# Performance work log

Measured on AMD Instinct MI355X. Metric: run time of the kernel, lower is better.

Reference implementation:

```python
import jax, jax.numpy as jnp
import numpy as np

WIN = 7
NP_ = WIN * WIN
COV_NORM = NP_ / (NP_ - 1)

def _box(x, w):
    # valid 7x7 box filter, NCHW, single channel
    return jax.lax.conv_general_dilated(
        x, w, window_strides=(1, 1), padding='VALID',
        dimension_numbers=('NCHW', 'OIHW', 'NCHW'))

def setup_inputs() -> dict:
    key = jax.random.key(0)
    k1, k2, k3, k4 = jax.random.split(key, 4)
    N, H, W = 64, 384, 384
    X = jax.random.uniform(k1, (N, 1, H, W), dtype=jnp.float32)
    Y = jax.random.uniform(k2, (N, 1, H, W), dtype=jnp.float32)
    norm = jax.random.uniform(k3, (N,), dtype=jnp.float32)
    mx = jax.random.uniform(k4, (N,), dtype=jnp.float32) + 0.5
    w = jnp.ones((1, 1, WIN, WIN), dtype=jnp.float32) / NP_
    return {"X": X, "Y": Y, "norm": norm, "max": mx, "w": w}

def reference(X, Y, norm, max, w):
    q = 100000.0
    X = X * q
    Y = Y * q
    mx = max * q
    data_range = mx[:, None, None, None]
    C1 = (0.01 * data_range) ** 2
    C2 = (0.03 * data_range) ** 2
    ux = _box(X, w)
    uy = _box(Y, w)
    uxx = _box(X * X, w)
    uyy = _box(Y * Y, w)
    uxy = _box(X * Y, w)
    vx = COV_NORM * (uxx - ux * ux)
    vy = COV_NORM * (uyy - uy * uy)
    vxy = COV_NORM * (uxy - ux * uy)
    A1 = 2 * ux * uy + C1
    A2 = 2 * vxy + C2
    B1 = ux ** 2 + uy ** 2 + C1
    B2 = vx + vy + C2
    S = (A1 * A2) / (B1 * B2)
    return -jnp.mean(S)
```

## Files before the change

### kernel.cpp

```cpp
#include <hip/hip_runtime.h>


constexpr int IND   = 384;
constexpr int OUTD  = 378;
constexpr int RB    = 14;
constexpr int BANDS = OUTD / RB;
constexpr int CPL   = 6;

using f32x2 = __attribute__((ext_vector_type(2))) float;

#define FMA2(a, b, c) __builtin_elementwise_fma((a), (b), (c))

__global__ __launch_bounds__(64, 2)
void ssim_band(const float* __restrict__ X, const float* __restrict__ Y,
               const float* __restrict__ MX, float* __restrict__ blocksum)
{
    const int band = blockIdx.x;
    const int n    = blockIdx.y;
    const int lane = threadIdx.x;
    const int c0   = lane * CPL;
    const int r0   = band * RB;

    const float* __restrict__ Xp = X + (size_t)n * (IND * IND) + c0;
    const float* __restrict__ Yp = Y + (size_t)n * (IND * IND) + c0;

    f32x2 hx[7][3], hy[7][3];
    f32x2 sx[3]  = {}, sy[3]  = {};
    f32x2 sxx[3] = {}, syy[3] = {}, sxy[3] = {};

#define LOADROW(DX, DY, R) {                                                  \
    const float* _px = Xp + (size_t)(R) * IND;                                \
    const float* _py = Yp + (size_t)(R) * IND;                                \
    DX[0] = *(const f32x2*)_px;                                               \
    DX[1] = *(const f32x2*)(_px + 2);                                         \
    DX[2] = *(const f32x2*)(_px + 4);                                         \
    DY[0] = *(const f32x2*)_py;                                               \
    DY[1] = *(const f32x2*)(_py + 2);                                         \
    DY[2] = *(const f32x2*)(_py + 4); }

#pragma unroll
    for (int k = 0; k < 7; ++k) LOADROW(hx[k], hy[k], r0 + k)

    f32x2 pax[3], pay[3], pbx[3], pby[3];
    LOADROW(pax, pay, r0 + 7)
    LOADROW(pbx, pby, r0 + 8)

#pragma unroll
    for (int k = 0; k < 7; ++k)
#pragma unroll
        for (int g = 0; g < 3; ++g) {
            f32x2 x = hx[k][g], y = hy[k][g];
            sx[g] += x;  sy[g] += y;
            sxx[g] = FMA2(x, x, sxx[g]);
            syy[g] = FMA2(y, y, syy[g]);
            sxy[g] = FMA2(x, y, sxy[g]);
        }

    const float m   = MX[n];
    const float c1s = (0.01f * m) * (0.01f * m);
    const float c2s = (0.03f * m) * (0.03f * m);
    const float k1  = 2401.0f * c1s;
    const float k2  = 2401.0f * c2s;
    const f32x2 K1  = {k1, k1};
    const f32x2 K2  = {k2, k2};
    const f32x2 CN  = {49.0f / 48.0f, 49.0f / 48.0f};
    const f32x2 CN2 = {2.0f * 49.0f / 48.0f, 2.0f * 49.0f / 48.0f};
    const f32x2 TWO = {2.0f, 2.0f};
    const f32x2 F49 = {49.0f, 49.0f};

#define EL(S, c) (((c) & 1) ? S[(c) >> 1].y : S[(c) >> 1].x)

#define HSUM(S, O) {                                                          \
    float _n0 = __shfl_down(EL(S,0), 1), _n1 = __shfl_down(EL(S,1), 1);       \
    float _n2 = __shfl_down(EL(S,2), 1), _n3 = __shfl_down(EL(S,3), 1);       \
    float _n4 = __shfl_down(EL(S,4), 1), _n5 = __shfl_down(EL(S,5), 1);       \
    float _t  = ((EL(S,0)+EL(S,1)) + (EL(S,2)+EL(S,3))) + (EL(S,4)+EL(S,5));  \
    O[0] = _t   + _n0;                                                        \
    O[1] = O[0] - EL(S,0) + _n1;                                              \
    O[2] = O[1] - EL(S,1) + _n2;                                              \
    O[3] = O[2] - EL(S,2) + _n3;                                              \
    O[4] = O[3] - EL(S,3) + _n4;                                              \
    O[5] = O[4] - EL(S,4) + _n5; }

    float partial = 0.f;

#pragma unroll 1
    for (int kk = 0; kk < RB / 7; ++kk) {
#pragma unroll
        for (int i = 0; i < 7; ++i) {
            float t1[6], t2[6], t34[6], t5[6];
            f32x2 u[3];
#pragma unroll
            for (int g = 0; g < 3; ++g) u[g] = sxx[g] + syy[g];
            HSUM(sx,  t1) HSUM(sy,  t2) HSUM(sxy, t5) HSUM(u, t34)

            if (lane < 63) {
#pragma unroll
                for (int g = 0; g < 3; ++g) {
                    f32x2 T1  = {t1[2*g],  t1[2*g+1]};
                    f32x2 T2  = {t2[2*g],  t2[2*g+1]};
                    f32x2 T5  = {t5[2*g],  t5[2*g+1]};
                    f32x2 T34 = {t34[2*g], t34[2*g+1]};
                    f32x2 pxy = T1 * T2;
                    f32x2 ss  = FMA2(T1, T1, T2 * T2);
                    f32x2 A1  = FMA2(TWO, pxy, K1);
                    f32x2 B1  = ss + K1;
                    f32x2 A2  = FMA2(CN2, FMA2(F49, T5, -pxy), K2);
                    f32x2 B2  = FMA2(CN,  FMA2(F49, T34, -ss), K2);
                    f32x2 num = A1 * A2;
                    f32x2 den = B1 * B2;
                    partial += __fdividef(num.x, den.x)
                             + __fdividef(num.y, den.y);
                }
            }

#pragma unroll
            for (int g = 0; g < 3; ++g) {
                f32x2 nx = pax[g], ny = pay[g];
                f32x2 ox = hx[i][g], oy = hy[i][g];
                sx[g] += nx - ox;
                sy[g] += ny - oy;
                sxx[g] = FMA2(nx, nx, FMA2(-ox, ox, sxx[g]));
                syy[g] = FMA2(ny, ny, FMA2(-oy, oy, syy[g]));
                sxy[g] = FMA2(nx, ny, FMA2(-ox, oy, sxy[g]));
                hx[i][g] = nx;  hy[i][g] = ny;
                pax[g] = pbx[g]; pay[g] = pby[g];
            }
            int nr = r0 + 7 * kk + i + 9;
            if (nr > IND - 1) nr = IND - 1;
            LOADROW(pbx, pby, nr)
        }
    }
#undef HSUM
#undef EL
#undef LOADROW

#pragma unroll
    for (int off = 32; off; off >>= 1) partial += __shfl_down(partial, off);
    if (lane == 0) blocksum[(size_t)n * BANDS + band] = partial;
}

__global__ __launch_bounds__(256)
void ssim_reduce(const float* __restrict__ blocksum, float* __restrict__ out,
                 int nblocks, float inv_npix)
{
    const int tid = threadIdx.x;
    float s = 0.f;
    for (int i = tid; i < nblocks; i += 256) s += blocksum[i];
#pragma unroll
    for (int off = 32; off; off >>= 1) s += __shfl_down(s, off);
    __shared__ float ws[4];
    if ((tid & 63) == 0) ws[tid >> 6] = s;
    __syncthreads();
    if (tid == 0) out[0] = -(ws[0] + ws[1] + ws[2] + ws[3]) * inv_npix;
}

extern "C" void kernel_launch(void* const* d_in, const int* in_sizes, int n_in,
                              void* d_out, int out_size, void* d_ws, size_t ws_size,
                              hipStream_t stream)
{
    const float* X  = (const float*)d_in[0];
    const float* Y  = (const float*)d_in[1];
    const float* MX = (const float*)d_in[3];

    const int N       = in_sizes[3];
    const int nblocks = N * BANDS;

    float* bs = (float*)d_ws;

    dim3 grid(BANDS, N);
    ssim_band<<<grid, 64, 0, stream>>>(X, Y, MX, bs);

    const float inv_npix = 1.0f / ((float)N * OUTD * OUTD);
    ssim_reduce<<<1, 256, 0, stream>>>(bs, (float*)d_out, nblocks, inv_npix);
}
```

Baseline: 29.09 us.

## Replace cross-lane shuffles with overlapping 12-column loads and reload-based row eviction

Each lane now loads a 12-column span, overlapping the neighbouring lane's columns, so the horizontal 7-tap sums are computed in registers without __shfl_down. The 7-row history held in registers is dropped. The row leaving the vertical window is re-read from memory (likely a cache hit) and subtracted, and sxx and syy are merged into a single accumulator. This removes 24 shuffles per output row and many history registers, at the cost of twice the vertical-accumulation arithmetic and about twice the global/cache load traffic.

```diff
diff --git a/kernel.cpp b/kernel.cpp
--- a/kernel.cpp
+++ b/kernel.cpp
@@ -6,9 +6,9 @@
 constexpr int RB    = 14;
 constexpr int BANDS = OUTD / RB;
 constexpr int CPL   = 6;
+constexpr int SPAN  = 12;
 
 using f32x2 = __attribute__((ext_vector_type(2))) float;
-
 #define FMA2(a, b, c) __builtin_elementwise_fma((a), (b), (c))
 
 __global__ __launch_bounds__(64, 2)
@@ -18,43 +18,56 @@
     const int band = blockIdx.x;
     const int n    = blockIdx.y;
     const int lane = threadIdx.x;
-    const int c0   = lane * CPL;
-    const int r0   = band * RB;
+    int cL = lane * CPL;
+    if (cL > IND - SPAN) cL = IND - SPAN;
+    const int r0 = band * RB;
 
-    const float* __restrict__ Xp = X + (size_t)n * (IND * IND) + c0;
-    const float* __restrict__ Yp = Y + (size_t)n * (IND * IND) + c0;
+    const float* __restrict__ Xp = X + (size_t)n * (IND * IND) + cL;
+    const float* __restrict__ Yp = Y + (size_t)n * (IND * IND) + cL;
 
-    f32x2 hx[7][3], hy[7][3];
-    f32x2 sx[3]  = {}, sy[3]  = {};
-    f32x2 sxx[3] = {}, syy[3] = {}, sxy[3] = {};
+    f32x2 sx[6] = {}, sy[6] = {}, sxy[6] = {}, su[6] = {};
+    f32x2 nax[6], nay[6], nbx[6], nby[6];
+    f32x2 oax[6], oay[6], obx[6], oby[6];
 
 #define LOADROW(DX, DY, R) {                                                  \
     const float* _px = Xp + (size_t)(R) * IND;                                \
     const float* _py = Yp + (size_t)(R) * IND;                                \
-    DX[0] = *(const f32x2*)_px;                                               \
-    DX[1] = *(const f32x2*)(_px + 2);                                         \
-    DX[2] = *(const f32x2*)(_px + 4);                                         \
-    DY[0] = *(const f32x2*)_py;                                               \
-    DY[1] = *(const f32x2*)(_py + 2);                                         \
-    DY[2] = *(const f32x2*)(_py + 4); }
+    DX[0] = *(const f32x2*)_px;        DX[1] = *(const f32x2*)(_px + 2);      \
+    DX[2] = *(const f32x2*)(_px + 4);  DX[3] = *(const f32x2*)(_px + 6);      \
+    DX[4] = *(const f32x2*)(_px + 8);  DX[5] = *(const f32x2*)(_px + 10);     \
+    DY[0] = *(const f32x2*)_py;        DY[1] = *(const f32x2*)(_py + 2);      \
+    DY[2] = *(const f32x2*)(_py + 4);  DY[3] = *(const f32x2*)(_py + 6);      \
+    DY[4] = *(const f32x2*)(_py + 8);  DY[5] = *(const f32x2*)(_py + 10); }
 
+#define ACC(RX, RY) {                                                         \
+    _Pragma("unroll")                                                         \
+    for (int g = 0; g < 6; ++g) {                                             \
+        f32x2 x = RX[g], y = RY[g];                                           \
+        sx[g] += x;  sy[g] += y;                                              \
+        sxy[g] = FMA2(x, y, sxy[g]);                                          \
+        su[g]  = FMA2(x, x, FMA2(y, y, su[g]));                               \
+    } }
+
+#define SUB(RX, RY) {                                                         \
+    _Pragma("unroll")                                                         \
+    for (int g = 0; g < 6; ++g) {                                             \
+        f32x2 x = RX[g], y = RY[g];                                           \
+        sx[g] -= x;  sy[g] -= y;                                              \
+        sxy[g] = FMA2(-x, y, sxy[g]);                                         \
+        su[g]  = FMA2(-x, x, FMA2(-y, y, su[g]));                             \
+    } }
+
+    LOADROW(oax, oay, r0 + 0)
+    LOADROW(obx, oby, r0 + 1)
+    ACC(oax, oay)
+    ACC(obx, oby)
 #pragma unroll
-    for (int k = 0; k < 7; ++k) LOADROW(hx[k], hy[k], r0 + k)
-
-    f32x2 pax[3], pay[3], pbx[3], pby[3];
-    LOADROW(pax, pay, r0 + 7)
-    LOADROW(pbx, pby, r0 + 8)
-
-#pragma unroll
-    for (int k = 0; k < 7; ++k)
-#pragma unroll
-        for (int g = 0; g < 3; ++g) {
-            f32x2 x = hx[k][g], y = hy[k][g];
-            sx[g] += x;  sy[g] += y;
-            sxx[g] = FMA2(x, x, sxx[g]);
-            syy[g] = FMA2(y, y, syy[g]);
-            sxy[g] = FMA2(x, y, sxy[g]);
-        }
+    for (int k = 2; k < 6; ++k) {
+        LOADROW(nax, nay, r0 + k)
+        ACC(nax, nay)
+    }
+    LOADROW(nax, nay, r0 + 6)
+    LOADROW(nbx, nby, r0 + 7)
 
     const float m   = MX[n];
     const float c1s = (0.01f * m) * (0.01f * m);
@@ -68,71 +81,61 @@
     const f32x2 TWO = {2.0f, 2.0f};
     const f32x2 F49 = {49.0f, 49.0f};
 
+    const bool valid = (lane < 63);
+    float partial = 0.f;
+
 #define EL(S, c) (((c) & 1) ? S[(c) >> 1].y : S[(c) >> 1].x)
 
-#define HSUM(S, O) {                                                          \
-    float _n0 = __shfl_down(EL(S,0), 1), _n1 = __shfl_down(EL(S,1), 1);       \
-    float _n2 = __shfl_down(EL(S,2), 1), _n3 = __shfl_down(EL(S,3), 1);       \
-    float _n4 = __shfl_down(EL(S,4), 1), _n5 = __shfl_down(EL(S,5), 1);       \
-    float _t  = ((EL(S,0)+EL(S,1)) + (EL(S,2)+EL(S,3))) + (EL(S,4)+EL(S,5));  \
-    O[0] = _t   + _n0;                                                        \
-    O[1] = O[0] - EL(S,0) + _n1;                                              \
-    O[2] = O[1] - EL(S,1) + _n2;                                              \
-    O[3] = O[2] - EL(S,2) + _n3;                                              \
-    O[4] = O[3] - EL(S,3) + _n4;                                              \
-    O[5] = O[4] - EL(S,4) + _n5; }
+#define HS(S, O) {                                                            \
+    float _t = ((EL(S,0) + EL(S,1)) + (EL(S,2) + EL(S,3)))                    \
+             + ((EL(S,4) + EL(S,5)) + EL(S,6));                               \
+    O[0] = _t;                                                                \
+    _t += EL(S,7)  - EL(S,0);  O[1] = _t;                                     \
+    _t += EL(S,8)  - EL(S,1);  O[2] = _t;                                     \
+    _t += EL(S,9)  - EL(S,2);  O[3] = _t;                                     \
+    _t += EL(S,10) - EL(S,3);  O[4] = _t;                                     \
+    _t += EL(S,11) - EL(S,4);  O[5] = _t; }
 
-    float partial = 0.f;
+#define STEP(NAX, NAY, OAX, OAY, OLDR, NEWR) {                                \
+        ACC(NAX, NAY)                                                         \
+        float t1[6], t2[6], t5[6], t34[6];                                    \
+        HS(sx,  t1) HS(sy,  t2) HS(sxy, t5) HS(su, t34)                       \
+        SUB(OAX, OAY)                                                         \
+        { int _r = (OLDR); LOADROW(OAX, OAY, _r) }                            \
+        { int _r = (NEWR); if (_r > IND - 1) _r = IND - 1;                    \
+          LOADROW(NAX, NAY, _r) }                                             \
+        if (valid) {                                                          \
+            _Pragma("unroll")                                                 \
+            for (int g = 0; g < 3; ++g) {                                     \
+                f32x2 T1  = {t1[2*g],  t1[2*g+1]};                            \
+                f32x2 T2  = {t2[2*g],  t2[2*g+1]};                            \
+                f32x2 T5  = {t5[2*g],  t5[2*g+1]};                            \
+                f32x2 T34 = {t34[2*g], t34[2*g+1]};                           \
+                f32x2 pxy = T1 * T2;                                          \
+                f32x2 ss  = FMA2(T1, T1, T2 * T2);                            \
+                f32x2 A1  = FMA2(TWO, pxy, K1);                               \
+                f32x2 B1  = ss + K1;                                          \
+                f32x2 A2  = FMA2(CN2, FMA2(F49, T5, -pxy), K2);               \
+                f32x2 B2  = FMA2(CN,  FMA2(F49, T34, -ss), K2);               \
+                f32x2 num = A1 * A2;                                          \
+                f32x2 den = B1 * B2;                                          \
+                partial += __fdividef(num.x, den.x)                           \
+                         + __fdividef(num.y, den.y);                          \
+            }                                                                 \
+        }                                                                     \
+    }
 
 #pragma unroll 1
-    for (int kk = 0; kk < RB / 7; ++kk) {
-#pragma unroll
-        for (int i = 0; i < 7; ++i) {
-            float t1[6], t2[6], t34[6], t5[6];
-            f32x2 u[3];
-#pragma unroll
-            for (int g = 0; g < 3; ++g) u[g] = sxx[g] + syy[g];
-            HSUM(sx,  t1) HSUM(sy,  t2) HSUM(sxy, t5) HSUM(u, t34)
-
-            if (lane < 63) {
-#pragma unroll
-                for (int g = 0; g < 3; ++g) {
-                    f32x2 T1  = {t1[2*g],  t1[2*g+1]};
-                    f32x2 T2  = {t2[2*g],  t2[2*g+1]};
-                    f32x2 T5  = {t5[2*g],  t5[2*g+1]};
-                    f32x2 T34 = {t34[2*g], t34[2*g+1]};
-                    f32x2 pxy = T1 * T2;
-                    f32x2 ss  = FMA2(T1, T1, T2 * T2);
-                    f32x2 A1  = FMA2(TWO, pxy, K1);
-                    f32x2 B1  = ss + K1;
-                    f32x2 A2  = FMA2(CN2, FMA2(F49, T5, -pxy), K2);
-                    f32x2 B2  = FMA2(CN,  FMA2(F49, T34, -ss), K2);
-                    f32x2 num = A1 * A2;
-                    f32x2 den = B1 * B2;
-                    partial += __fdividef(num.x, den.x)
-                             + __fdividef(num.y, den.y);
-                }
-            }
-
-#pragma unroll
-            for (int g = 0; g < 3; ++g) {
-                f32x2 nx = pax[g], ny = pay[g];
-                f32x2 ox = hx[i][g], oy = hy[i][g];
-                sx[g] += nx - ox;
-                sy[g] += ny - oy;
-                sxx[g] = FMA2(nx, nx, FMA2(-ox, ox, sxx[g]));
-                syy[g] = FMA2(ny, ny, FMA2(-oy, oy, syy[g]));
-                sxy[g] = FMA2(nx, ny, FMA2(-ox, oy, sxy[g]));
-                hx[i][g] = nx;  hy[i][g] = ny;
-                pax[g] = pbx[g]; pay[g] = pby[g];
-            }
-            int nr = r0 + 7 * kk + i + 9;
-            if (nr > IND - 1) nr = IND - 1;
-            LOADROW(pbx, pby, nr)
-        }
+    for (int ii = 0; ii < RB / 2; ++ii) {
+        const int s0 = 2 * ii, s1 = 2 * ii + 1;
+        STEP(nax, nay, oax, oay, r0 + s0 + 2, r0 + s0 + 8)
+        STEP(nbx, nby, obx, oby, r0 + s1 + 2, r0 + s1 + 8)
     }
-#undef HSUM
+#undef STEP
+#undef HS
 #undef EL
+#undef SUB
+#undef ACC
 #undef LOADROW
 
 #pragma unroll
```

Result: slower. 35.53 us (+22.2%).
